# Performance work log

Measured on AMD Instinct MI355X. Metric: run time of the kernel, lower is better.

The kernel has to match this reference:

```python
import jax, jax.numpy as jnp
import numpy as np

UNITS = 1024
IN_DIM = 512
BATCH = 64
SEQ = 512


def setup_inputs() -> dict:
    key = jax.random.key(0)
    k1, k2, k3, k4 = jax.random.split(key, 4)
    x = jax.random.normal(k1, (BATCH, SEQ, IN_DIM), dtype=jnp.float32)
    # Keras LSTM params: kernel [D,4U], recurrent_kernel [U,4U], bias [4U]; gate order i,f,c,o
    Wx = jax.random.normal(k2, (IN_DIM, 4 * UNITS), dtype=jnp.float32) * (1.0 / np.sqrt(IN_DIM))
    Wh = jax.random.normal(k3, (UNITS, 4 * UNITS), dtype=jnp.float32) * (1.0 / np.sqrt(UNITS))
    b = jnp.zeros((4 * UNITS,), dtype=jnp.float32).at[UNITS:2 * UNITS].set(1.0)  # unit_forget_bias
    return {"x": x, "Wx": Wx, "Wh": Wh, "b": b}


def reference(x, Wx, Wh, b):
    B, T, D = x.shape
    U = Wh.shape[0]
    # Precompute input projections for all timesteps in one GEMM: [B,T,4U]
    gx = jnp.einsum('btd,dg->btg', x, Wx) + b
    gx = jnp.swapaxes(gx, 0, 1)  # [T,B,4U] for scan

    def step(carry, gx_t):
        h, c = carry
        g = gx_t + h @ Wh  # [B,4U]
        i, f, cc, o = jnp.split(g, 4, axis=-1)
        i = jax.nn.sigmoid(i)
        f = jax.nn.sigmoid(f)
        o = jax.nn.sigmoid(o)
        c_new = f * c + i * jnp.tanh(cc)
        h_new = o * jnp.tanh(c_new)
        return (h_new, c_new), None

    h0 = jnp.zeros((B, U), dtype=x.dtype)
    c0 = jnp.zeros((B, U), dtype=x.dtype)
    (h, c), _ = jax.lax.scan(step, (h0, c0), gx)
    # Keras return_state LSTM: pred (last output) == h_state
    return jnp.concatenate([h, h, c], axis=-1)
```

## Files before the change

kernel.cpp:

```cpp
#include <hip/hip_runtime.h>
#include <stdint.h>

#define T_STEPS 512
#define RING 16
#define SLOT_SHORTS 65536

typedef short short8 __attribute__((ext_vector_type(8)));
typedef float f32x16 __attribute__((ext_vector_type(16)));

#define OFF_DONE 0
#define DONE_BYTES (512 * 2 * 4 * 64)
#define OFF_HRING DONE_BYTES
#define OFF_XF (OFF_HRING + RING * SLOT_SHORTS * 2)
#define XF_BYTES (512 * 2 * 4 * 8 * 64 * 8 * 2)
#define OFF_WPACK (OFF_XF + XF_BYTES)
#define MEMSET_BYTES (OFF_HRING + SLOT_SHORTS * 2)

#define W_STR 1544
#define G_STR 36

__device__ __forceinline__ unsigned short f2bf(float f) {
  unsigned u = __float_as_uint(f);
  u += 0x7fffu + ((u >> 16) & 1u);
  return (unsigned short)(u >> 16);
}

__global__ __launch_bounds__(256) void k_xpack(const float* __restrict__ x,
                                               unsigned short* __restrict__ xf) {
  int o = blockIdx.x * 256 + threadIdx.x;
  int lane = o & 63;
  int kk = (o >> 6) & 7;
  int ks = (o >> 9) & 3;
  int g = (o >> 11) & 1;
  int t = o >> 12;
  int n = lane & 31, hh = lane >> 5;
  const float* src = x + (((size_t)(g * 32 + n) * 512 + t) * 512 +
                          ks * 128 + kk * 16 + hh * 8);
  float4 v0 = *(const float4*)src;
  float4 v1 = *(const float4*)(src + 4);
  short8 w;
  w[0] = (short)f2bf(v0.x); w[1] = (short)f2bf(v0.y);
  w[2] = (short)f2bf(v0.z); w[3] = (short)f2bf(v0.w);
  w[4] = (short)f2bf(v1.x); w[5] = (short)f2bf(v1.y);
  w[6] = (short)f2bf(v1.z); w[7] = (short)f2bf(v1.w);
  *(short8*)(xf + (size_t)o * 8) = w;
}

__global__ __launch_bounds__(256) void k_wpack(const float* __restrict__ Wx,
                                               const float* __restrict__ Wh,
                                               unsigned short* __restrict__ wp) {
  __shared__ unsigned short tile[64 * 68];
  int tid = threadIdx.x, lane = tid & 63, wave = tid >> 6;
  int kt = blockIdx.x >> 6;
  int ct = blockIdx.x & 63;
  int K0 = kt * 64, C0 = ct * 64;
  const float* src = (K0 < 512) ? (Wx + (size_t)K0 * 4096)
                                : (Wh + (size_t)(K0 - 512) * 4096);
  #pragma unroll
  for (int i = 0; i < 16; ++i) {
    int kl = i * 4 + wave;
    float v = src[(size_t)kl * 4096 + C0 + lane];
    tile[lane * 68 + kl] = f2bf(v);
  }
  __syncthreads();
  #pragma unroll
  for (int i = 0; i < 16; ++i) {
    int c = i * 4 + wave;
    int col = C0 + c;
    int gg = col >> 10, idx = col & 1023;
    int cp = (idx >> 3) * 32 + gg * 8 + (idx & 7);
    wp[(size_t)cp * 1536 + K0 + lane] = tile[c * 68 + lane];
  }
}

__global__ __launch_bounds__(256, 1) void k_scan(
    const unsigned short* __restrict__ xf,
    const unsigned short* __restrict__ wp,
    const float* __restrict__ bias,
    float* __restrict__ out,
    unsigned* __restrict__ done,
    unsigned short* __restrict__ hring) {
  __shared__ __align__(16) unsigned short Wlds[32 * W_STR];
  __shared__ float Gs[4][32 * G_STR];

  const int tid = threadIdx.x;
  const int lane = tid & 63;
  const int ks = tid >> 6;
  const int bid = blockIdx.x;
  const int g = bid & 1;
  const int cb = bid >> 1;
  const int cohort = cb >> 4;
  const int n = lane & 31;
  const int hh = lane >> 5;

  for (int i = tid; i < 32 * 192; i += 256) {
    int row = i / 192, o = i % 192;
    *(short8*)&Wlds[row * W_STR + o * 8] =
        *(const short8*)&wp[((size_t)cb * 32 + row) * 1536 + o * 8];
  }

  const int m = tid >> 3, uu = tid & 7;
  const int ug = cb * 8 + uu;
  const float bi = bias[ug], bff = bias[1024 + ug];
  const float bc_ = bias[2048 + ug], bo = bias[3072 + ug];
  float c_state = 0.f;
  const int ksp = cb >> 5, kkp = (cb >> 1) & 15, hhp = cb & 1;
  __syncthreads();

  const unsigned short* wb = &Wlds[n * W_STR + hh * 8];

  #pragma unroll 1
  for (int t = 0; t < T_STEPS; ++t) {
    f32x16 acc;
    #pragma unroll
    for (int r = 0; r < 16; ++r) acc[r] = 0.f;

    {
      const unsigned short* xs =
          xf + ((((size_t)t * 2 + g) * 4 + ks) * 8) * 512 + lane * 8;
      #pragma unroll
      for (int kk = 0; kk < 8; ++kk) {
        short8 xa = *(const short8*)(xs + kk * 512);
        short8 b = *(const short8*)(wb + ks * 128 + kk * 16);
        acc = __builtin_amdgcn_mfma_f32_32x32x16_bf16(xa, b, acc, 0, 0, 0);
      }
    }

    if (t > 0 && lane == 0) {
      const unsigned long long* dp = (const unsigned long long*)(
          done + (((size_t)(t - 1) * 2 + g) * 4 + ks) * 16);
      float burn = c_state + 1.0f;
      while (__hip_atomic_load(dp, __ATOMIC_RELAXED,
                               __HIP_MEMORY_SCOPE_AGENT) != 0x0000001000000010ULL) {
        #pragma unroll
        for (int i = 0; i < 64; ++i)
          burn = __builtin_fmaf(burn, 1.0000001f, 1e-30f);
      }
      asm volatile("" :: "v"(burn));
    }
    __builtin_amdgcn_fence(__ATOMIC_ACQUIRE, "workgroup");
    if (t > 0 && (t & (RING - 1)) == 0)
      __builtin_amdgcn_fence(__ATOMIC_ACQUIRE, "agent");

    {
      const unsigned short* hs = hring + (size_t)(t & (RING - 1)) * SLOT_SHORTS +
                                 ((g * 4 + ks) * 16) * 512 + lane * 8;
      short8 ha[16];
      #pragma unroll
      for (int kk = 0; kk < 16; ++kk)
        ha[kk] = *(const short8*)(hs + kk * 512);
      #pragma unroll
      for (int kk = 0; kk < 16; ++kk) {
        short8 b = *(const short8*)(wb + 512 + ks * 256 + kk * 16);
        acc = __builtin_amdgcn_mfma_f32_32x32x16_bf16(ha[kk], b, acc, 0, 0, 0);
      }
    }

    #pragma unroll
    for (int r = 0; r < 16; ++r) {
      int row = (r & 3) + 8 * (r >> 2) + 4 * hh;
      Gs[ks][row * G_STR + n] = acc[r];
    }
    __syncthreads();

    float sI = bi, sF = bff, sC = bc_, sO = bo;
    #pragma unroll
    for (int w = 0; w < 4; ++w) {
      sI += Gs[w][m * G_STR + uu];
      sF += Gs[w][m * G_STR + 8 + uu];
      sC += Gs[w][m * G_STR + 16 + uu];
      sO += Gs[w][m * G_STR + 24 + uu];
    }
    float ig = 1.f / (1.f + __expf(-sI));
    float fg = 1.f / (1.f + __expf(-sF));
    float og = 1.f / (1.f + __expf(-sO));
    float cb2 = tanhf(sC);
    c_state = fg * c_state + ig * cb2;
    float h = og * tanhf(c_state);

    unsigned hv = (unsigned)f2bf(h);
    unsigned o1 = (unsigned)__shfl_xor((int)hv, 1, 64);
    unsigned lo = hv | (o1 << 16);
    unsigned long long hi = (unsigned long long)(unsigned)__shfl_xor((int)lo, 2, 64);
    unsigned long long v64 = ((unsigned long long)lo) | (hi << 32);
    if ((uu & 3) == 0) {
      unsigned short* hdst = hring + (size_t)((t + 1) & (RING - 1)) * SLOT_SHORTS +
                             ((g * 4 + ksp) * 16 + kkp) * 512 +
                             (hhp * 32 + m) * 8 + uu;
      __hip_atomic_store((unsigned long long*)hdst, v64,
                         __ATOMIC_RELAXED, __HIP_MEMORY_SCOPE_AGENT);
    }
    if (t == T_STEPS - 1) {
      float* orow = out + (size_t)(g * 32 + m) * 3072 + ug;
      orow[0] = h;
      orow[1024] = h;
      orow[2048] = c_state;
    }
    __syncthreads();
    if (tid == 0)
      __hip_atomic_fetch_add(
          done + (((size_t)t * 2 + g) * 4 + (cohort >> 1)) * 16 + (cohort & 1),
          1u, __ATOMIC_RELAXED, __HIP_MEMORY_SCOPE_AGENT);
  }
}

extern "C" void kernel_launch(void* const* d_in, const int* in_sizes, int n_in,
                              void* d_out, int out_size, void* d_ws, size_t ws_size,
                              hipStream_t stream) {
  const float* x  = (const float*)d_in[0];
  const float* Wx = (const float*)d_in[1];
  const float* Wh = (const float*)d_in[2];
  const float* b  = (const float*)d_in[3];
  float* out = (float*)d_out;
  char* ws = (char*)d_ws;
  unsigned* done = (unsigned*)(ws + OFF_DONE);
  unsigned short* hring = (unsigned short*)(ws + OFF_HRING);
  unsigned short* xf = (unsigned short*)(ws + OFF_XF);
  unsigned short* wp = (unsigned short*)(ws + OFF_WPACK);

  hipMemsetAsync(d_ws, 0, MEMSET_BYTES, stream);
  k_xpack<<<8192, 256, 0, stream>>>(x, xf);
  k_wpack<<<1536, 256, 0, stream>>>(Wx, Wh, wp);

  void* args[] = {(void*)&xf, (void*)&wp, (void*)&b, (void*)&out, (void*)&done,
                  (void*)&hring};
  hipLaunchCooperativeKernel((void*)k_scan, dim3(256), dim3(256), args, 0, stream);
}
```

Baseline: 2.292 ms.

## Replace per-step counter barrier with epoch flags and prefetch next input projection

Each block now publishes its completed step as a monotonically increasing epoch flag, and waiting waves poll the 32 producer flags in parallel across lanes with s_sleep. This replaces the single per-step atomic counter that lane 0 spun on with an FMA burn loop. The input-projection MFMAs for step t+1 are moved to the end of step t, so they overlap the barrier wait rather than sitting on the critical path after it. A vmcnt wait before publishing the flag, and a fallback to a normal launch if the cooperative launch fails, are also added. The risk is extra polling traffic from many lanes and slightly more work before the flag is published.

```diff
diff --git a/kernel.cpp b/kernel.cpp
--- a/kernel.cpp
+++ b/kernel.cpp
@@ -8,9 +8,9 @@
 typedef short short8 __attribute__((ext_vector_type(8)));
 typedef float f32x16 __attribute__((ext_vector_type(16)));
 
-#define OFF_DONE 0
-#define DONE_BYTES (512 * 2 * 4 * 64)
-#define OFF_HRING DONE_BYTES
+#define OFF_EP 0
+#define EP_BYTES (512 * 2 * 4 * 64)
+#define OFF_HRING EP_BYTES
 #define OFF_XF (OFF_HRING + RING * SLOT_SHORTS * 2)
 #define XF_BYTES (512 * 2 * 4 * 8 * 64 * 8 * 2)
 #define OFF_WPACK (OFF_XF + XF_BYTES)
@@ -78,7 +78,7 @@
     const unsigned short* __restrict__ wp,
     const float* __restrict__ bias,
     float* __restrict__ out,
-    unsigned* __restrict__ done,
+    unsigned* __restrict__ ep,
     unsigned short* __restrict__ hring) {
   __shared__ __align__(16) unsigned short Wlds[32 * W_STR];
   __shared__ float Gs[4][32 * G_STR];
@@ -89,7 +89,6 @@
   const int bid = blockIdx.x;
   const int g = bid & 1;
   const int cb = bid >> 1;
-  const int cohort = cb >> 4;
   const int n = lane & 31;
   const int hh = lane >> 5;
 
@@ -109,34 +108,29 @@
 
   const unsigned short* wb = &Wlds[n * W_STR + hh * 8];
 
+  f32x16 acc;
+  #pragma unroll
+  for (int r = 0; r < 16; ++r) acc[r] = 0.f;
+  {
+    const unsigned short* xs = xf + ((size_t)(g * 4 + ks) * 8) * 512 + lane * 8;
+    #pragma unroll
+    for (int kk = 0; kk < 8; ++kk) {
+      short8 xa = *(const short8*)(xs + kk * 512);
+      short8 b = *(const short8*)(wb + ks * 128 + kk * 16);
+      acc = __builtin_amdgcn_mfma_f32_32x32x16_bf16(xa, b, acc, 0, 0, 0);
+    }
+  }
+
   #pragma unroll 1
   for (int t = 0; t < T_STEPS; ++t) {
-    f32x16 acc;
-    #pragma unroll
-    for (int r = 0; r < 16; ++r) acc[r] = 0.f;
-
-    {
-      const unsigned short* xs =
-          xf + ((((size_t)t * 2 + g) * 4 + ks) * 8) * 512 + lane * 8;
-      #pragma unroll
-      for (int kk = 0; kk < 8; ++kk) {
-        short8 xa = *(const short8*)(xs + kk * 512);
-        short8 b = *(const short8*)(wb + ks * 128 + kk * 16);
-        acc = __builtin_amdgcn_mfma_f32_32x32x16_bf16(xa, b, acc, 0, 0, 0);
+    if (t > 0) {
+      const unsigned* dp = ep + ((size_t)g * 128 + ks * 32 + (lane & 31)) * 4;
+      for (;;) {
+        unsigned v = __hip_atomic_load(dp, __ATOMIC_RELAXED,
+                                       __HIP_MEMORY_SCOPE_AGENT);
+        if (__all((int)(v >= (unsigned)t))) break;
+        __builtin_amdgcn_s_sleep(1);
       }
-    }
-
-    if (t > 0 && lane == 0) {
-      const unsigned long long* dp = (const unsigned long long*)(
-          done + (((size_t)(t - 1) * 2 + g) * 4 + ks) * 16);
-      float burn = c_state + 1.0f;
-      while (__hip_atomic_load(dp, __ATOMIC_RELAXED,
-                               __HIP_MEMORY_SCOPE_AGENT) != 0x0000001000000010ULL) {
-        #pragma unroll
-        for (int i = 0; i < 64; ++i)
-          burn = __builtin_fmaf(burn, 1.0000001f, 1e-30f);
-      }
-      asm volatile("" :: "v"(burn));
     }
     __builtin_amdgcn_fence(__ATOMIC_ACQUIRE, "workgroup");
     if (t > 0 && (t & (RING - 1)) == 0)
@@ -196,24 +190,41 @@
       orow[1024] = h;
       orow[2048] = c_state;
     }
+
+    f32x16 acc2;
+    #pragma unroll
+    for (int r = 0; r < 16; ++r) acc2[r] = 0.f;
+    {
+      int tx = (t + 1) & (T_STEPS - 1);
+      const unsigned short* xs =
+          xf + ((((size_t)tx * 2 + g) * 4 + ks) * 8) * 512 + lane * 8;
+      #pragma unroll
+      for (int kk = 0; kk < 8; ++kk) {
+        short8 xa = *(const short8*)(xs + kk * 512);
+        short8 b = *(const short8*)(wb + ks * 128 + kk * 16);
+        acc2 = __builtin_amdgcn_mfma_f32_32x32x16_bf16(xa, b, acc2, 0, 0, 0);
+      }
+    }
+    asm volatile("s_waitcnt vmcnt(0)" ::: "memory");
     __syncthreads();
     if (tid == 0)
-      __hip_atomic_fetch_add(
-          done + (((size_t)t * 2 + g) * 4 + (cohort >> 1)) * 16 + (cohort & 1),
-          1u, __ATOMIC_RELAXED, __HIP_MEMORY_SCOPE_AGENT);
+      __hip_atomic_store(ep + ((size_t)g * 128 + cb) * 4, (unsigned)(t + 1),
+                         __ATOMIC_RELAXED, __HIP_MEMORY_SCOPE_AGENT);
+    acc = acc2;
   }
 }
 
 extern "C" void kernel_launch(void* const* d_in, const int* in_sizes, int n_in,
                               void* d_out, int out_size, void* d_ws, size_t ws_size,
                               hipStream_t stream) {
+  (void)in_sizes; (void)n_in; (void)out_size; (void)ws_size;
   const float* x  = (const float*)d_in[0];
   const float* Wx = (const float*)d_in[1];
   const float* Wh = (const float*)d_in[2];
   const float* b  = (const float*)d_in[3];
   float* out = (float*)d_out;
   char* ws = (char*)d_ws;
-  unsigned* done = (unsigned*)(ws + OFF_DONE);
+  unsigned* ep = (unsigned*)(ws + OFF_EP);
   unsigned short* hring = (unsigned short*)(ws + OFF_HRING);
   unsigned short* xf = (unsigned short*)(ws + OFF_XF);
   unsigned short* wp = (unsigned short*)(ws + OFF_WPACK);
@@ -222,7 +233,11 @@
   k_xpack<<<8192, 256, 0, stream>>>(x, xf);
   k_wpack<<<1536, 256, 0, stream>>>(Wx, Wh, wp);
 
-  void* args[] = {(void*)&xf, (void*)&wp, (void*)&b, (void*)&out, (void*)&done,
+  void* args[] = {(void*)&xf, (void*)&wp, (void*)&b, (void*)&out, (void*)&ep,
                   (void*)&hring};
-  hipLaunchCooperativeKernel((void*)k_scan, dim3(256), dim3(256), args, 0, stream);
-}
+  hipError_t e = hipLaunchCooperativeKernel((void*)k_scan, dim3(256), dim3(256),
+                                            args, 0, stream);
+  if (e != hipSuccess) {
+    k_scan<<<dim3(256), dim3(256), 0, stream>>>(xf, wp, b, out, ep, hring);
+  }
+}
```

Result: slower. 2.984 ms (+30.2%).
